# Performance work log

Measured on AMD Instinct MI355X. Metric: run time of the kernel, lower is better.

Reference implementation:

```python
import jax, jax.numpy as jnp
import numpy as np
import math

B, S, HID = 2, 2048, 4096
NH, NKV, HD = 32, 8, 128
ROPE_BASE = 10000.0


def _rope_tables(b, s, hd):
    inv_freq = 1.0 / (ROPE_BASE ** (jnp.arange(0, hd, 2, dtype=jnp.float32) / hd))
    t = jnp.arange(s, dtype=jnp.float32)
    freqs = jnp.outer(t, inv_freq)            # [s, hd/2]
    emb = jnp.concatenate([freqs, freqs], -1)  # [s, hd]
    cos = jnp.broadcast_to(jnp.cos(emb)[None], (b, s, hd))
    sin = jnp.broadcast_to(jnp.sin(emb)[None], (b, s, hd))
    return cos, sin


def setup_inputs() -> dict:
    key = jax.random.key(0)
    ks = jax.random.split(key, 5)
    hidden_states = jax.random.normal(ks[0], (B, S, HID), dtype=jnp.float32)
    # additive causal mask [B,1,S,S]: 0 on/below diagonal, large negative above
    causal = jnp.tril(jnp.ones((S, S), dtype=bool))
    attention_mask = jnp.where(causal, 0.0, jnp.finfo(jnp.float32).min)[None, None]
    attention_mask = jnp.broadcast_to(attention_mask, (B, 1, S, S)).astype(jnp.float32)
    cos, sin = _rope_tables(B, S, HD)
    sc = 0.02
    Wq = jax.random.normal(ks[1], (NH * HD, HID), dtype=jnp.float32) * sc
    Wk = jax.random.normal(ks[2], (NKV * HD, HID), dtype=jnp.float32) * sc
    Wv = jax.random.normal(ks[3], (NKV * HD, HID), dtype=jnp.float32) * sc
    Wo = jax.random.normal(ks[4], (HID, NH * HD), dtype=jnp.float32) * sc
    return {"hidden_states": hidden_states, "attention_mask": attention_mask,
            "cos": cos, "sin": sin, "Wq": Wq, "Wk": Wk, "Wv": Wv, "Wo": Wo}


def _rotate_half(x):
    x1, x2 = jnp.split(x, 2, axis=-1)
    return jnp.concatenate([-x2, x1], axis=-1)


def reference(hidden_states, attention_mask, cos, sin, Wq, Wk, Wv, Wo):
    b, s, _ = hidden_states.shape
    # projections (nn.Linear: x @ W.T, no bias)
    q = jnp.einsum('bsh,oh->bso', hidden_states, Wq).reshape(b, s, NH, HD).transpose(0, 2, 1, 3)
    k = jnp.einsum('bsh,oh->bso', hidden_states, Wk).reshape(b, s, NKV, HD).transpose(0, 2, 1, 3)
    v = jnp.einsum('bsh,oh->bso', hidden_states, Wv).reshape(b, s, NKV, HD).transpose(0, 2, 1, 3)
    # RoPE (cos/sin: [b,s,hd] -> unsqueeze head dim)
    c, sn = cos[:, None], sin[:, None]
    q = q * c + _rotate_half(q) * sn
    k = k * c + _rotate_half(k) * sn
    # repeat_kv: [b,nkv,s,d] -> [b,nh,s,d] (repeat_interleave over head dim)
    n_rep = NH // NKV
    k = jnp.repeat(k, n_rep, axis=1)
    v = jnp.repeat(v, n_rep, axis=1)
    # eager attention
    scores = jnp.einsum('bhqd,bhkd->bhqk', q, k) / math.sqrt(HD)
    scores = scores + attention_mask[:, :, :, :k.shape[2]]
    probs = jax.nn.softmax(scores.astype(jnp.float32), axis=-1).astype(q.dtype)
    attn = jnp.einsum('bhqk,bhkd->bhqd', probs, v)
    attn = attn.transpose(0, 2, 1, 3).reshape(b, s, NH * HD)
    return jnp.einsum('bso,ho->bsh', attn, Wo)
```

## Files before the change

kernel.cpp:

```cpp
#include <hip/hip_runtime.h>
#include <hip/hip_bf16.h>
#include <cstdint>

#define S_LEN 2048
#define HIDDEN 4096
#define NH 32
#define NKV 8
#define HD 128
#define BATCH 2
#define MROWS (BATCH * S_LEN)

typedef float f32x4 __attribute__((ext_vector_type(4)));
typedef __bf16 bf16x8 __attribute__((ext_vector_type(8)));
typedef __bf16 bf16x4 __attribute__((ext_vector_type(4)));

static __device__ inline f32x4 mfma16(bf16x8 a, bf16x8 b, f32x4 c) {
    return __builtin_amdgcn_mfma_f32_16x16x32_bf16(a, b, c, 0, 0, 0);
}

static __device__ inline void gl_lds16(const __bf16* g, __bf16* l) {
    __builtin_amdgcn_global_load_lds(
        (const __attribute__((address_space(1))) void*)g,
        (__attribute__((address_space(3))) void*)l, 16, 0, 0);
}

#define LGKM0()  asm volatile("s_waitcnt lgkmcnt(0)" ::: "memory")
#define SCHEDB() __builtin_amdgcn_sched_barrier(0)
#define SBAR()   __builtin_amdgcn_s_barrier()

__global__ __launch_bounds__(256) void conv_f32_bf16(const float* __restrict__ in,
                                                     __bf16* __restrict__ out, int n8) {
    int i = blockIdx.x * 256 + threadIdx.x;
    if (i >= n8) return;
    const float4* p = (const float4*)in + (size_t)i * 2;
    float4 a = p[0], b = p[1];
    bf16x8 v;
    v[0] = (__bf16)a.x; v[1] = (__bf16)a.y; v[2] = (__bf16)a.z; v[3] = (__bf16)a.w;
    v[4] = (__bf16)b.x; v[5] = (__bf16)b.y; v[6] = (__bf16)b.z; v[7] = (__bf16)b.w;
    ((bf16x8*)out)[i] = v;
}

template<int MODE, int BM>
__global__ __launch_bounds__(512, 2) void gemm256(const __bf16* __restrict__ A,
                                                  const __bf16* __restrict__ B,
                                                  float* __restrict__ Cf,
                                                  __bf16* __restrict__ Qo,
                                                  __bf16* __restrict__ Ko,
                                                  __bf16* __restrict__ Vo,
                                                  int N, int K, int nbx) {
    constexpr int MF = BM / 32;
    constexpr int MH = BM / 64;
    __shared__ __bf16 As[2][BM * 64];
    __shared__ __bf16 Bs[2][256 * 64];
    const int tid = threadIdx.x, lane = tid & 63;
    const int lq = lane & 15, hi2 = lane >> 4;
    const int wv = tid >> 6;
    const int wr = wv >> 2, wc = wv & 3;

    const int cpx = gridDim.x >> 3;
    const int bid = blockIdx.x;
    const int swz = (bid & 7) * cpx + (bid >> 3);
    const int bx = swz % nbx, by = swz / nbx;
    const int brow = by * BM, bcol = bx * 256;

    f32x4 acc[MF][4] = {};
    bf16x8 af[MH][2], bfr[2][2];
    const int NT = K >> 6;

    auto stageA = [&](int bb, int kt, int roff) {
        #pragma unroll
        for (int r = 0; r < 2; ++r) {
            int i = r * 512 + tid;
            int row = i >> 3, sl = i & 7, lsl = sl ^ (row & 7);
            gl_lds16(A + (size_t)(brow + roff + row) * K + kt * 64 + lsl * 8,
                     &As[bb][roff * 64 + i * 8]);
        }
    };
    auto stageB = [&](int bb, int kt, int roff) {
        #pragma unroll
        for (int r = 0; r < 2; ++r) {
            int i = r * 512 + tid;
            int row = i >> 3, sl = i & 7, lsl = sl ^ (row & 7);
            gl_lds16(B + (size_t)(bcol + roff + row) * K + kt * 64 + lsl * 8,
                     &Bs[bb][roff * 64 + i * 8]);
        }
    };
    auto loadA = [&](int bb, int mq) {
        #pragma unroll
        for (int mi = 0; mi < MH; ++mi) {
            int row = wr * (BM / 2) + (mq * MH + mi) * 16 + lq;
            #pragma unroll
            for (int kk = 0; kk < 2; ++kk) {
                int lsl = (kk * 4 + hi2) ^ (row & 7);
                af[mi][kk] = *(const bf16x8*)&As[bb][row * 64 + lsl * 8];
            }
        }
    };
    auto loadB = [&](int bb, int nq) {
        #pragma unroll
        for (int ni = 0; ni < 2; ++ni) {
            int row = wc * 64 + (nq * 2 + ni) * 16 + lq;
            #pragma unroll
            for (int kk = 0; kk < 2; ++kk) {
                int lsl = (kk * 4 + hi2) ^ (row & 7);
                bfr[ni][kk] = *(const bf16x8*)&Bs[bb][row * 64 + lsl * 8];
            }
        }
    };
    auto mmaq = [&](int mq, int nq) {
        __builtin_amdgcn_s_setprio(1);
        #pragma unroll
        for (int kk = 0; kk < 2; ++kk)
            #pragma unroll
            for (int mi = 0; mi < MH; ++mi)
                #pragma unroll
                for (int ni = 0; ni < 2; ++ni)
                    acc[mq * MH + mi][nq * 2 + ni] =
                        mfma16(af[mi][kk], bfr[ni][kk], acc[mq * MH + mi][nq * 2 + ni]);
        __builtin_amdgcn_s_setprio(0);
    };

    stageA(0, 0, 0);
    if constexpr (BM == 256) stageA(0, 0, 128);
    stageB(0, 0, 0);
    stageB(0, 0, 128);

    for (int t = 0; t < NT; ++t) {
        const int cur = t & 1, nxt = cur ^ 1;
        const int tn = (t + 1 < NT) ? t + 1 : NT - 1;
        stageA(nxt, tn, 0);
        if constexpr (BM == 256) stageA(nxt, tn, 128);
        stageB(nxt, tn, 0);
        if constexpr (BM == 256) { asm volatile("s_waitcnt vmcnt(6)" ::: "memory"); }
        else                     { asm volatile("s_waitcnt vmcnt(4)" ::: "memory"); }
        SBAR(); SCHEDB();
        loadA(cur, 0); loadB(cur, 0);
        LGKM0(); SCHEDB();
        mmaq(0, 0);
        SBAR(); SCHEDB();
        loadB(cur, 1);
        stageB(nxt, tn, 128);
        SBAR(); SCHEDB();
        LGKM0(); SCHEDB();
        mmaq(0, 1);
        SBAR(); SCHEDB();
        loadA(cur, 1);
        SBAR(); SCHEDB();
        LGKM0(); SCHEDB();
        mmaq(1, 1);
        SBAR(); SCHEDB();
        loadB(cur, 0);
        SBAR(); SCHEDB();
        LGKM0(); SCHEDB();
        mmaq(1, 0);
        SBAR(); SCHEDB();
    }

    #pragma unroll
    for (int m = 0; m < MF; ++m) {
        #pragma unroll
        for (int n = 0; n < 4; ++n) {
            int row0 = brow + wr * (BM / 2) + m * 16 + (hi2 << 2);
            int col  = bcol + wc * 64 + n * 16 + lq;
            if constexpr (MODE == 3) {
                if (col < NKV * HD) {
                    #pragma unroll
                    for (int j = 0; j < 4; ++j)
                        Ko[(size_t)(row0 + j) * (NKV * HD) + col] = (__bf16)acc[m][n][j];
                } else {
                    int c2 = col - NKV * HD;
                    int hkv = c2 >> 7, d = c2 & (HD - 1);
                    int bb2 = row0 >> 11, s = row0 & (S_LEN - 1);
                    bf16x4 t4;
                    #pragma unroll
                    for (int j = 0; j < 4; ++j) t4[j] = (__bf16)acc[m][n][j];
                    *(bf16x4*)&Vo[((size_t)((bb2 * NKV + hkv) * HD + d)) * S_LEN + s] = t4;
                }
            } else if constexpr (MODE == 1) {
                #pragma unroll
                for (int j = 0; j < 4; ++j)
                    Cf[(size_t)(row0 + j) * N + col] = acc[m][n][j];
            } else {
                #pragma unroll
                for (int j = 0; j < 4; ++j)
                    Qo[(size_t)(row0 + j) * N + col] = (__bf16)acc[m][n][j];
            }
        }
    }
}

__global__ __launch_bounds__(256) void rope_kernel(__bf16* __restrict__ X,
                                                   const float* __restrict__ ct,
                                                   const float* __restrict__ st,
                                                   int nheads, int total) {
    int idx = blockIdx.x * 256 + threadIdx.x;
    if (idx >= total) return;
    int d  = idx & 63;
    int hh = (idx >> 6) % nheads;
    int m  = idx / (64 * nheads);
    __bf16* p = X + (size_t)m * (nheads * HD) + hh * HD;
    float c = ct[(size_t)m * HD + d];
    float s = st[(size_t)m * HD + d];
    float x1 = (float)p[d], x2 = (float)p[d + 64];
    p[d]      = (__bf16)(x1 * c - x2 * s);
    p[d + 64] = (__bf16)(x2 * c + x1 * s);
}

__global__ __launch_bounds__(256, 3) void attn_kernel(const __bf16* __restrict__ Q,
                                                      const __bf16* __restrict__ K,
                                                      const __bf16* __restrict__ V,
                                                      __bf16* __restrict__ O) {
    constexpr int QB = 128, KB = 32;
    constexpr int nqb = S_LEN / QB;
    const int cpx = gridDim.x >> 3;
    const int b0 = blockIdx.x;
    const int bid = (b0 & 7) * cpx + (b0 >> 3);
    const int pair = bid & 7;
    const int h    = (bid >> 3) & (NH - 1);
    const int b    = bid >> 8;
    const int hkv = h >> 2;
    const int tid = threadIdx.x, lane = tid & 63, w = tid >> 6;
    const int lq = lane & 15, hi2 = lane >> 4;

    __shared__ __bf16 Ks[2][KB * HD];
    __shared__ __bf16 Vt[2][HD * KB];
    __shared__ __bf16 Pl[4][2][16][40];

    const int qbA = nqb - 1 - pair;
    const int nkbA = 4 * (qbA + 1);
    const int T = nkbA + 4 * (pair + 1);

    auto stage = [&](int bb, int k0s) {
        #pragma unroll
        for (int r = 0; r < 2; ++r) {
            int i = r * 256 + tid;
            {   int row = i >> 4, sl = i & 15, lsl = sl ^ (row & 7);
                gl_lds16(&K[((size_t)(b * S_LEN + k0s + row)) * (NKV * HD) + hkv * HD + lsl * 8],
                         &Ks[bb][i * 8]); }
            {   int d = i >> 2, sl = i & 3, lsl = sl ^ (d & 3);
                gl_lds16(&V[((size_t)((b * NKV + hkv) * HD + d)) * S_LEN + k0s + lsl * 8],
                         &Vt[bb][i * 8]); }
        }
    };

    const float c2 = 0.08838834764831843f * 1.4426950408889634f;

    stage(0, 0);
    int tt = 0;
    #pragma unroll 1
    for (int pass = 0; pass < 2; ++pass) {
        const int qb = pass ? pair : qbA;
        const int q0 = qb * QB, qrow_lo = q0 + w * 32;
        const int nkb = 4 * (qb + 1);

        bf16x8 qf[2][4];
        #pragma unroll
        for (int mt = 0; mt < 2; ++mt) {
            int row = qrow_lo + mt * 16 + lq;
            const __bf16* qp = Q + ((size_t)(b * S_LEN + row)) * (NH * HD) + h * HD + hi2 * 8;
            #pragma unroll
            for (int c = 0; c < 4; ++c) {
                bf16x8 v = *(const bf16x8*)(qp + c * 32);
                #pragma unroll
                for (int e = 0; e < 8; ++e) v[e] = (__bf16)((float)v[e] * c2);
                qf[mt][c] = v;
            }
        }

        f32x4 o_acc[2][8] = {};
        float m_r[2] = {-1e30f, -1e30f}, l_r[2] = {0.f, 0.f};

        #pragma unroll 1
        for (int kb = 0; kb < nkb; ++kb, ++tt) {
            int tn = (tt + 1 < T) ? tt + 1 : T - 1;
            int k0n = (tn < nkbA ? tn : tn - nkbA) * KB;
            stage((tt + 1) & 1, k0n);
            asm volatile("s_waitcnt vmcnt(4)" ::: "memory");
            SBAR(); SCHEDB();
            const int cur = tt & 1;
            const int k0  = kb * KB;
            const __bf16* ks = &Ks[cur][0];
            const __bf16* vt = &Vt[cur][0];

            f32x4 sc[2][2] = {};
            #pragma unroll
            for (int t = 0; t < 2; ++t) {
                int krow = t * 16 + lq;
                #pragma unroll
                for (int c = 0; c < 4; ++c) {
                    int psl = (c * 4 + hi2) ^ (krow & 7);
                    bf16x8 kf = *(const bf16x8*)&ks[krow * HD + psl * 8];
                    sc[0][t] = mfma16(kf, qf[0][c], sc[0][t]);
                    sc[1][t] = mfma16(kf, qf[1][c], sc[1][t]);
                }
            }

            #pragma unroll
            for (int mt = 0; mt < 2; ++mt) {
                int q_abs = qrow_lo + mt * 16 + lq;
                if (k0 + KB - 1 > qrow_lo + mt * 16) {
                    #pragma unroll
                    for (int t = 0; t < 2; ++t)
                        #pragma unroll
                        for (int j = 0; j < 4; ++j) {
                            int kv_abs = k0 + t * 16 + hi2 * 4 + j;
                            if (kv_abs > q_abs) sc[mt][t][j] = -1e30f;
                        }
                }
                float pmax = fmaxf(
                    fmaxf(fmaxf(sc[mt][0][0], sc[mt][0][1]), fmaxf(sc[mt][0][2], sc[mt][0][3])),
                    fmaxf(fmaxf(sc[mt][1][0], sc[mt][1][1]), fmaxf(sc[mt][1][2], sc[mt][1][3])));
                pmax = fmaxf(pmax, __shfl_xor(pmax, 16));
                pmax = fmaxf(pmax, __shfl_xor(pmax, 32));
                if (!__all(pmax - m_r[mt] <= 8.0f)) {
                    float mn = fmaxf(m_r[mt], pmax);
                    float sf = __builtin_amdgcn_exp2f(m_r[mt] - mn);
                    m_r[mt] = mn;
                    l_r[mt] *= sf;
                    #pragma unroll
                    for (int dt = 0; dt < 8; ++dt)
                        #pragma unroll
                        for (int j = 0; j < 4; ++j) o_acc[mt][dt][j] *= sf;
                }
                float rs = 0.f;
                #pragma unroll
                for (int t = 0; t < 2; ++t)
                    #pragma unroll
                    for (int j = 0; j < 4; ++j) {
                        float p = __builtin_amdgcn_exp2f(sc[mt][t][j] - m_r[mt]);
                        sc[mt][t][j] = p;
                        rs += p;
                    }
                rs += __shfl_xor(rs, 16);
                rs += __shfl_xor(rs, 32);
                l_r[mt] += rs;
                #pragma unroll
                for (int t = 0; t < 2; ++t) {
                    bf16x4 pw;
                    #pragma unroll
                    for (int j = 0; j < 4; ++j) pw[j] = (__bf16)sc[mt][t][j];
                    *(bf16x4*)&Pl[w][mt][lq][t * 16 + hi2 * 4] = pw;
                }
            }

            LGKM0(); SCHEDB();
            bf16x8 pf0 = *(const bf16x8*)&Pl[w][0][lq][hi2 * 8];
            bf16x8 pf1 = *(const bf16x8*)&Pl[w][1][lq][hi2 * 8];

            #pragma unroll
            for (int dt = 0; dt < 8; ++dt) {
                int vrow = dt * 16 + lq;
                int psl  = hi2 ^ (vrow & 3);
                bf16x8 vf = *(const bf16x8*)&vt[vrow * KB + psl * 8];
                o_acc[0][dt] = mfma16(vf, pf0, o_acc[0][dt]);
                o_acc[1][dt] = mfma16(vf, pf1, o_acc[1][dt]);
            }
            LGKM0(); SCHEDB();
            SBAR(); SCHEDB();
        }

        #pragma unroll
        for (int mt = 0; mt < 2; ++mt) {
            float inv = 1.0f / l_r[mt];
            int q_abs = qrow_lo + mt * 16 + lq;
            __bf16* op = O + ((size_t)(b * S_LEN + q_abs)) * (NH * HD) + h * HD;
            #pragma unroll
            for (int dt = 0; dt < 8; ++dt) {
                bf16x4 t4;
                #pragma unroll
                for (int j = 0; j < 4; ++j) t4[j] = (__bf16)(o_acc[mt][dt][j] * inv);
                *(bf16x4*)&op[dt * 16 + hi2 * 4] = t4;
            }
        }
    }
}

extern "C" void kernel_launch(void* const* d_in, const int* in_sizes, int n_in,
                              void* d_out, int out_size, void* d_ws, size_t ws_size,
                              hipStream_t stream) {
    const float* X  = (const float*)d_in[0];
    const float* ct = (const float*)d_in[2];
    const float* st = (const float*)d_in[3];
    const float* Wq = (const float*)d_in[4];
    const float* Wk = (const float*)d_in[5];
    const float* Wv = (const float*)d_in[6];
    const float* Wo = (const float*)d_in[7];
    float* out = (float*)d_out;

    const size_t MEL  = (size_t)MROWS * HIDDEN;
    const size_t KVEL = (size_t)MROWS * (NKV * HD);
    const int NQKV = NH * HD + 2 * NKV * HD;

    __bf16* Wqkv = (__bf16*)d_ws;
    __bf16* Xb   = Wqkv + (size_t)NQKV * HIDDEN;
    __bf16* Qb   = Xb + MEL;
    __bf16* Kb   = Qb + MEL;
    __bf16* VtG  = Kb + KVEL;
    __bf16* Ab   = Wqkv;
    __bf16* Wob  = Xb;

    dim3 blk(256);
    hipLaunchKernelGGL(conv_f32_bf16, dim3((int)(MEL / 8 / 256)), blk, 0, stream, X,  Xb, (int)(MEL / 8));
    hipLaunchKernelGGL(conv_f32_bf16, dim3((int)(MEL / 8 / 256)), blk, 0, stream, Wq, Wqkv, (int)(MEL / 8));
    hipLaunchKernelGGL(conv_f32_bf16, dim3((int)(KVEL / 8 / 256)), blk, 0, stream,
                       Wk, Wqkv + (size_t)HIDDEN * HIDDEN, (int)(KVEL / 8));
    hipLaunchKernelGGL(conv_f32_bf16, dim3((int)(KVEL / 8 / 256)), blk, 0, stream,
                       Wv, Wqkv + (size_t)(HIDDEN + NKV * HD) * HIDDEN, (int)(KVEL / 8));

    hipLaunchKernelGGL((gemm256<0, 256>), dim3(256), dim3(512), 0, stream,
                       Xb, Wqkv, nullptr, Qb, nullptr, nullptr, NH * HD, HIDDEN, 16);
    hipLaunchKernelGGL((gemm256<3, 128>), dim3(256), dim3(512), 0, stream,
                       Xb, Wqkv + (size_t)HIDDEN * HIDDEN, nullptr, nullptr, Kb, VtG,
                       2 * NKV * HD, HIDDEN, 8);

    hipLaunchKernelGGL(rope_kernel, dim3((MROWS * NH * 64) / 256), blk, 0, stream,
                       Qb, ct, st, NH, MROWS * NH * 64);
    hipLaunchKernelGGL(rope_kernel, dim3((MROWS * NKV * 64) / 256), blk, 0, stream,
                       Kb, ct, st, NKV, MROWS * NKV * 64);

    hipLaunchKernelGGL(conv_f32_bf16, dim3((int)(MEL / 8 / 256)), blk, 0, stream, Wo, Wob, (int)(MEL / 8));

    hipLaunchKernelGGL(attn_kernel, dim3(512), blk, 0, stream, Qb, Kb, VtG, Ab);

    hipLaunchKernelGGL((gemm256<1, 256>), dim3(256), dim3(512), 0, stream,
                       Ab, Wob, out, nullptr, nullptr, nullptr, HIDDEN, HIDDEN, 16);
}
```

Baseline: 586.6 us.

## Restructure GEMM main loop into k-split phases with split B staging buffers

The GEMM inner loop now iterates over the two k-halves of each 64-wide tile separately, loading all A fragments for one kk at a time and running MFMAs on each N half. The B tile is split into two separately staged 128-row halves so each half's next-tile prefetch can be issued between compute phases. This cuts the number of barriers per iteration and changes the vmcnt wait points. The aim is better overlap of global-to-LDS loads with MFMA work and fewer stalls. In exchange, register pressure and correctness of the wait counts and the B row remapping carry risk.

```diff
diff --git a/kernel.cpp b/kernel.cpp
--- a/kernel.cpp
+++ b/kernel.cpp
@@ -25,6 +25,7 @@
 }
 
 #define LGKM0()  asm volatile("s_waitcnt lgkmcnt(0)" ::: "memory")
+#define VMC(n)   asm volatile("s_waitcnt vmcnt(" #n ")" ::: "memory")
 #define SCHEDB() __builtin_amdgcn_sched_barrier(0)
 #define SBAR()   __builtin_amdgcn_s_barrier()
 
@@ -41,17 +42,16 @@
 }
 
 template<int MODE, int BM>
-__global__ __launch_bounds__(512, 2) void gemm256(const __bf16* __restrict__ A,
-                                                  const __bf16* __restrict__ B,
-                                                  float* __restrict__ Cf,
-                                                  __bf16* __restrict__ Qo,
-                                                  __bf16* __restrict__ Ko,
-                                                  __bf16* __restrict__ Vo,
-                                                  int N, int K, int nbx) {
+__global__ __launch_bounds__(512, 2) void gemm8p(const __bf16* __restrict__ A,
+                                                 const __bf16* __restrict__ B,
+                                                 float* __restrict__ Cf,
+                                                 __bf16* __restrict__ Qo,
+                                                 __bf16* __restrict__ Ko,
+                                                 __bf16* __restrict__ Vo,
+                                                 int N, int K, int nbx) {
     constexpr int MF = BM / 32;
-    constexpr int MH = BM / 64;
     __shared__ __bf16 As[2][BM * 64];
-    __shared__ __bf16 Bs[2][256 * 64];
+    __shared__ __bf16 Bs[2][2][128 * 64];
     const int tid = threadIdx.x, lane = tid & 63;
     const int lq = lane & 15, hi2 = lane >> 4;
     const int wv = tid >> 6;
@@ -64,7 +64,7 @@
     const int brow = by * BM, bcol = bx * 256;
 
     f32x4 acc[MF][4] = {};
-    bf16x8 af[MH][2], bfr[2][2];
+    bf16x8 af[MF], bfr[2];
     const int NT = K >> 6;
 
     auto stageA = [&](int bb, int kt, int roff) {
@@ -76,84 +76,72 @@
                      &As[bb][roff * 64 + i * 8]);
         }
     };
-    auto stageB = [&](int bb, int kt, int roff) {
+    auto stageBP = [&](int bb, int kt, int nq) {
         #pragma unroll
         for (int r = 0; r < 2; ++r) {
             int i = r * 512 + tid;
-            int row = i >> 3, sl = i & 7, lsl = sl ^ (row & 7);
-            gl_lds16(B + (size_t)(bcol + roff + row) * K + kt * 64 + lsl * 8,
-                     &Bs[bb][roff * 64 + i * 8]);
-        }
-    };
-    auto loadA = [&](int bb, int mq) {
-        #pragma unroll
-        for (int mi = 0; mi < MH; ++mi) {
-            int row = wr * (BM / 2) + (mq * MH + mi) * 16 + lq;
-            #pragma unroll
-            for (int kk = 0; kk < 2; ++kk) {
-                int lsl = (kk * 4 + hi2) ^ (row & 7);
-                af[mi][kk] = *(const bf16x8*)&As[bb][row * 64 + lsl * 8];
-            }
-        }
-    };
-    auto loadB = [&](int bb, int nq) {
+            int rowp = i >> 3, sl = i & 7, lsl = sl ^ (rowp & 7);
+            int grow = bcol + ((rowp >> 5) << 6) + nq * 32 + (rowp & 31);
+            gl_lds16(B + (size_t)grow * K + kt * 64 + lsl * 8,
+                     &Bs[bb][nq][i * 8]);
+        }
+    };
+    auto loadA = [&](int bb, int kk) {
+        #pragma unroll
+        for (int mi = 0; mi < MF; ++mi) {
+            int row = wr * (BM / 2) + mi * 16 + lq;
+            int lsl = (kk * 4 + hi2) ^ (row & 7);
+            af[mi] = *(const bf16x8*)&As[bb][row * 64 + lsl * 8];
+        }
+    };
+    auto loadB = [&](int bb, int nq, int kk) {
         #pragma unroll
         for (int ni = 0; ni < 2; ++ni) {
-            int row = wc * 64 + (nq * 2 + ni) * 16 + lq;
-            #pragma unroll
-            for (int kk = 0; kk < 2; ++kk) {
-                int lsl = (kk * 4 + hi2) ^ (row & 7);
-                bfr[ni][kk] = *(const bf16x8*)&Bs[bb][row * 64 + lsl * 8];
-            }
-        }
-    };
-    auto mmaq = [&](int mq, int nq) {
+            int rowp = wc * 32 + ni * 16 + lq;
+            int lsl = (kk * 4 + hi2) ^ (rowp & 7);
+            bfr[ni] = *(const bf16x8*)&Bs[bb][nq][rowp * 64 + lsl * 8];
+        }
+    };
+    auto mma = [&](int nq) {
         __builtin_amdgcn_s_setprio(1);
         #pragma unroll
-        for (int kk = 0; kk < 2; ++kk)
-            #pragma unroll
-            for (int mi = 0; mi < MH; ++mi)
-                #pragma unroll
-                for (int ni = 0; ni < 2; ++ni)
-                    acc[mq * MH + mi][nq * 2 + ni] =
-                        mfma16(af[mi][kk], bfr[ni][kk], acc[mq * MH + mi][nq * 2 + ni]);
+        for (int mi = 0; mi < MF; ++mi)
+            #pragma unroll
+            for (int ni = 0; ni < 2; ++ni)
+                acc[mi][nq * 2 + ni] = mfma16(af[mi], bfr[ni], acc[mi][nq * 2 + ni]);
         __builtin_amdgcn_s_setprio(0);
     };
 
     stageA(0, 0, 0);
     if constexpr (BM == 256) stageA(0, 0, 128);
-    stageB(0, 0, 0);
-    stageB(0, 0, 128);
+    stageBP(0, 0, 0);
+    stageBP(0, 0, 1);
 
     for (int t = 0; t < NT; ++t) {
         const int cur = t & 1, nxt = cur ^ 1;
         const int tn = (t + 1 < NT) ? t + 1 : NT - 1;
+        VMC(2);
+        SBAR(); SCHEDB();
         stageA(nxt, tn, 0);
         if constexpr (BM == 256) stageA(nxt, tn, 128);
-        stageB(nxt, tn, 0);
-        if constexpr (BM == 256) { asm volatile("s_waitcnt vmcnt(6)" ::: "memory"); }
-        else                     { asm volatile("s_waitcnt vmcnt(4)" ::: "memory"); }
+        loadA(cur, 0); loadB(cur, 0, 0);
+        LGKM0(); SCHEDB();
+        mma(0);
+        if constexpr (BM == 256) { VMC(4); } else { VMC(2); }
         SBAR(); SCHEDB();
-        loadA(cur, 0); loadB(cur, 0);
+        stageBP(nxt, tn, 0);
+        loadB(cur, 1, 0);
         LGKM0(); SCHEDB();
-        mmaq(0, 0);
+        mma(1);
         SBAR(); SCHEDB();
-        loadB(cur, 1);
-        stageB(nxt, tn, 128);
+        stageBP(nxt, tn, 1);
+        loadA(cur, 1); loadB(cur, 0, 1);
+        LGKM0(); SCHEDB();
+        mma(0);
         SBAR(); SCHEDB();
+        loadB(cur, 1, 1);
         LGKM0(); SCHEDB();
-        mmaq(0, 1);
-        SBAR(); SCHEDB();
-        loadA(cur, 1);
-        SBAR(); SCHEDB();
-        LGKM0(); SCHEDB();
-        mmaq(1, 1);
-        SBAR(); SCHEDB();
-        loadB(cur, 0);
-        SBAR(); SCHEDB();
-        LGKM0(); SCHEDB();
-        mmaq(1, 0);
-        SBAR(); SCHEDB();
+        mma(1);
     }
 
     #pragma unroll
@@ -407,9 +395,9 @@
     hipLaunchKernelGGL(conv_f32_bf16, dim3((int)(KVEL / 8 / 256)), blk, 0, stream,
                        Wv, Wqkv + (size_t)(HIDDEN + NKV * HD) * HIDDEN, (int)(KVEL / 8));
 
-    hipLaunchKernelGGL((gemm256<0, 256>), dim3(256), dim3(512), 0, stream,
+    hipLaunchKernelGGL((gemm8p<0, 256>), dim3(256), dim3(512), 0, stream,
                        Xb, Wqkv, nullptr, Qb, nullptr, nullptr, NH * HD, HIDDEN, 16);
-    hipLaunchKernelGGL((gemm256<3, 128>), dim3(256), dim3(512), 0, stream,
+    hipLaunchKernelGGL((gemm8p<3, 128>), dim3(256), dim3(512), 0, stream,
                        Xb, Wqkv + (size_t)HIDDEN * HIDDEN, nullptr, nullptr, Kb, VtG,
                        2 * NKV * HD, HIDDEN, 8);
 
@@ -422,6 +410,6 @@
 
     hipLaunchKernelGGL(attn_kernel, dim3(512), blk, 0, stream, Qb, Kb, VtG, Ab);
 
-    hipLaunchKernelGGL((gemm256<1, 256>), dim3(256), dim3(512), 0, stream,
+    hipLaunchKernelGGL((gemm8p<1, 256>), dim3(256), dim3(512), 0, stream,
                        Ab, Wob, out, nullptr, nullptr, nullptr, HIDDEN, HIDDEN, 16);
 }
```

Result: slower. 621.7 us (+6.0%).
